# Performance work log

Measured on AMD Instinct MI355X. Metric: run time of the kernel, lower is better.

The kernel has to match this reference:

```python
import jax, jax.numpy as jnp
import numpy as np

H, N, L, BATCH = 128, 64, 4096, 8


def _make_dplr_hippo(n):
    # HiPPO-LegS -> NPLR -> DPLR diagonalization (float64 numpy, as in torch source)
    ar = np.arange(n, dtype=np.float64)
    p0 = np.sqrt(1.0 + 2.0 * ar)
    A = p0[:, None] * p0[None, :]
    A = np.tril(A) - np.diag(ar)
    nhippo = -A
    Pv = np.sqrt(ar + 0.5)
    Bv = np.sqrt(2.0 * ar + 1.0)
    S = nhippo + Pv[:, None] * Pv[None, :]
    Lambda_real = np.mean(np.diag(S)) * np.ones(n)
    Lambda_imag, V = np.linalg.eigh(S * -1j)
    V = V.astype(np.complex64)
    P = (V.conj().T @ Pv.astype(np.complex64))
    B = (V.conj().T @ Bv.astype(np.complex64))
    Lam = (Lambda_real + 1j * Lambda_imag).astype(np.complex64)
    return Lam, P, B


def _ri(x):  # complex -> [..., 2] real view (like torch.view_as_real)
    return np.stack([x.real, x.imag], axis=-1).astype(np.float32)


def setup_inputs() -> dict:
    key = jax.random.key(0)
    k_u, k_c, k_d = jax.random.split(key, 3)
    Lam, P, B = _make_dplr_hippo(N)
    Lambda_ri = np.tile(_ri(Lam)[None], (H, 1, 1))          # [H, N, 2]
    P_ri = np.tile(_ri(P)[None], (H, 1, 1))                 # [H, N, 2]
    B_ri = np.tile(_ri(B)[None], (H, 1, 1))                 # [H, N, 2]
    C_ri = jax.random.normal(k_c, (H, N, 2), dtype=jnp.float32)
    D = jax.random.normal(k_d, (H, 1), dtype=jnp.float32)
    u = jax.random.normal(k_u, (BATCH, L, H), dtype=jnp.float32)
    step = jnp.array([1.0 / L], dtype=jnp.float32)
    return {
        "u": u,
        "B_ri": jnp.asarray(B_ri),
        "C_ri": jnp.asarray(C_ri),
        "D": D,
        "Lambda_ri": jnp.asarray(Lambda_ri),
        "P_ri": jnp.asarray(P_ri),
        "step": step,
    }


def _as_c(x_ri):
    return jax.lax.complex(x_ri[..., 0], x_ri[..., 1])


def reference(u, B_ri, C_ri, D, Lambda_ri, P_ri, step):
    Bc = _as_c(B_ri)        # [H, N] complex64
    Cc = _as_c(C_ri)        # [H, N]
    Lam = _as_c(Lambda_ri)  # [H, N]
    Pc = _as_c(P_ri)        # [H, N]
    batch, seq_len, h = u.shape

    # roots of unity and bilinear-transform terms
    z = jnp.exp(-2j * jnp.pi * jnp.arange(seq_len) / seq_len)   # [L] complex64
    g = (2.0 / step).astype(jnp.complex64) * ((1.0 - z) / (1.0 + z))  # [L]
    c = 2.0 / (1.0 + z)                                          # [L]

    # Cauchy resolvent, shared by the four cauchy_dot reductions: [H, L, N]
    r = 1.0 / (g[None, :, None] - Lam[:, None, :])

    def cauchy(v):  # v: [H, N] -> [H, L]
        return jnp.einsum("hn,hln->hl", v, r)

    k00 = cauchy(jnp.conj(Cc) * Bc)
    k01 = cauchy(jnp.conj(Cc) * Pc)
    k10 = cauchy(jnp.conj(Pc) * Bc)
    k11 = cauchy(jnp.conj(Pc) * Pc)
    at_roots = c[None, :] * (k00 - k01 * (1.0 / (1.0 + k11)) * k10)  # [H, L]

    kernel = jnp.fft.ifft(at_roots, n=seq_len, axis=-1).real  # [H, L] float32

    # linear (full) FFT convolution, length 2L-1, keep first L samples
    nfft = 2 * seq_len - 1
    u_f = jnp.fft.rfft(u, n=nfft, axis=1)                 # [B, F, H]
    k_f = jnp.fft.rfft(kernel, n=nfft, axis=-1)           # [H, F]
    y = jnp.fft.irfft(u_f * k_f.T[None], n=nfft, axis=1)[:, :seq_len, :]  # [B, L, H]

    return y + u @ D  # D: [H,1] -> broadcast add of skip term
```

## Files before the change

kernel.cpp:

```cpp
#include <hip/hip_runtime.h>
#include <hip/hip_bf16.h>
#include <math.h>

#define HH 128
#define NN 64
#define LL 4096
#define BB 8
#define NFFT 8192
#define KSTR 4160

#define CAU_BLOCKS 1024
#define TRU_BLOCKS 4096
#define SKP_BLOCKS 8192

__device__ __forceinline__ float2 cmul(float2 a, float2 b) {
    return make_float2(a.x * b.x - a.y * b.y, a.x * b.y + a.y * b.x);
}
__device__ __forceinline__ float2 cadd(float2 a, float2 b) {
    return make_float2(a.x + b.x, a.y + b.y);
}
__device__ __forceinline__ float2 csub(float2 a, float2 b) {
    return make_float2(a.x - b.x, a.y - b.y);
}
__device__ __forceinline__ int brev13(int x) { return (int)(__brev((unsigned)x) >> 19); }
__device__ __forceinline__ int kkmap(int t) {
    return (t < 4096) ? (((t & 63) << 6) | (t >> 6)) : 4096;
}
__device__ __forceinline__ int swz(int v) { return v ^ ((v >> 4) & 15); }

__device__ __forceinline__ float2 twid(float rev, float sg) {
    return make_float2(__builtin_amdgcn_cosf(rev), sg * __builtin_amdgcn_sinf(rev));
}


template <int M>
__device__ __forceinline__ void dif_f8(float2* d, int N, int tid, int nt, float sg) {
    const float inv2m = 1.0f / (2.0f * (float)M);
    const float inv4m = 1.0f / (4.0f * (float)M);
    const float inv8m = 1.0f / (8.0f * (float)M);
    const float s2 = 0.70710678118654752f;
    for (int q = tid; q < (N >> 3); q += nt) {
        int j = q & (M - 1);
        int i0 = ((q & ~(M - 1)) << 3) + j;
        float2 x0 = d[swz(i0)],         x1 = d[swz(i0 + M)],
               x2 = d[swz(i0 + 2 * M)], x3 = d[swz(i0 + 3 * M)],
               x4 = d[swz(i0 + 4 * M)], x5 = d[swz(i0 + 5 * M)],
               x6 = d[swz(i0 + 6 * M)], x7 = d[swz(i0 + 7 * M)];
        float jf = (float)j;
        float2 w8 = twid(jf * inv8m, sg);
        float2 w4 = twid(jf * inv4m, sg);
        float2 w2 = twid(jf * inv2m, sg);
        float2 e1 = make_float2(s2, sg * s2);
        float2 e3 = make_float2(-s2, sg * s2);
        float2 y0 = cadd(x0, x4), y1 = cadd(x1, x5), y2 = cadd(x2, x6), y3 = cadd(x3, x7);
        float2 t0 = csub(x0, x4), t1 = csub(x1, x5), t2 = csub(x2, x6), t3 = csub(x3, x7);
        float2 w8i = make_float2(-sg * w8.y, sg * w8.x);
        float2 z0 = cmul(w8, t0);
        float2 z1 = cmul(cmul(w8, e1), t1);
        float2 z2 = cmul(w8i, t2);
        float2 z3 = cmul(cmul(w8, e3), t3);
        {
            float2 a0 = cadd(y0, y2);
            float2 a2 = cmul(w4, csub(y0, y2));
            float2 a1 = cadd(y1, y3);
            float2 t = cmul(w4, csub(y1, y3));
            float2 a3 = make_float2(-sg * t.y, sg * t.x);
            d[swz(i0)]         = cadd(a0, a1);
            d[swz(i0 + M)]     = cmul(w2, csub(a0, a1));
            d[swz(i0 + 2 * M)] = cadd(a2, a3);
            d[swz(i0 + 3 * M)] = cmul(w2, csub(a2, a3));
        }
        {
            float2 a0 = cadd(z0, z2);
            float2 a2 = cmul(w4, csub(z0, z2));
            float2 a1 = cadd(z1, z3);
            float2 t = cmul(w4, csub(z1, z3));
            float2 a3 = make_float2(-sg * t.y, sg * t.x);
            d[swz(i0 + 4 * M)] = cadd(a0, a1);
            d[swz(i0 + 5 * M)] = cmul(w2, csub(a0, a1));
            d[swz(i0 + 6 * M)] = cadd(a2, a3);
            d[swz(i0 + 7 * M)] = cmul(w2, csub(a2, a3));
        }
    }
    __syncthreads();
}

template <int M>
__device__ __forceinline__ void dit_f8(float2* d, int N, int tid, int nt, float sg) {
    const float inv2m = 1.0f / (2.0f * (float)M);
    const float inv4m = 1.0f / (4.0f * (float)M);
    const float inv8m = 1.0f / (8.0f * (float)M);
    const float s2 = 0.70710678118654752f;
    for (int q = tid; q < (N >> 3); q += nt) {
        int j = q & (M - 1);
        int i0 = ((q & ~(M - 1)) << 3) + j;
        float2 x0 = d[swz(i0)],         x1 = d[swz(i0 + M)],
               x2 = d[swz(i0 + 2 * M)], x3 = d[swz(i0 + 3 * M)],
               x4 = d[swz(i0 + 4 * M)], x5 = d[swz(i0 + 5 * M)],
               x6 = d[swz(i0 + 6 * M)], x7 = d[swz(i0 + 7 * M)];
        float jf = (float)j;
        float2 wA = twid(jf * inv2m, sg);
        float2 wB = twid(jf * inv4m, sg);
        float2 wC = twid(jf * inv8m, sg);
        float2 t;
        t = cmul(wA, x1); float2 b0 = cadd(x0, t), b1 = csub(x0, t);
        t = cmul(wA, x3); float2 b2 = cadd(x2, t), b3 = csub(x2, t);
        t = cmul(wA, x5); float2 b4 = cadd(x4, t), b5 = csub(x4, t);
        t = cmul(wA, x7); float2 b6 = cadd(x6, t), b7 = csub(x6, t);
        float2 wBi = make_float2(-sg * wB.y, sg * wB.x);
        t = cmul(wB, b2);  float2 c0 = cadd(b0, t), c2 = csub(b0, t);
        t = cmul(wBi, b3); float2 c1 = cadd(b1, t), c3 = csub(b1, t);
        t = cmul(wB, b6);  float2 c4 = cadd(b4, t), c6 = csub(b4, t);
        t = cmul(wBi, b7); float2 c5 = cadd(b5, t), c7 = csub(b5, t);
        float2 e1 = make_float2(s2, sg * s2);
        float2 e3 = make_float2(-s2, sg * s2);
        float2 w1 = cmul(wC, e1);
        float2 w2_ = make_float2(-sg * wC.y, sg * wC.x);
        float2 w3 = cmul(wC, e3);
        t = cmul(wC, c4);  d[swz(i0)]         = cadd(c0, t); d[swz(i0 + 4 * M)] = csub(c0, t);
        t = cmul(w1, c5);  d[swz(i0 + M)]     = cadd(c1, t); d[swz(i0 + 5 * M)] = csub(c1, t);
        t = cmul(w2_, c6); d[swz(i0 + 2 * M)] = cadd(c2, t); d[swz(i0 + 6 * M)] = csub(c2, t);
        t = cmul(w3, c7);  d[swz(i0 + 3 * M)] = cadd(c3, t); d[swz(i0 + 7 * M)] = csub(c3, t);
    }
    __syncthreads();
}

__global__ __launch_bounds__(256, 8) void stage1_kernel(
    const float* __restrict__ u,
    const float* __restrict__ B_ri, const float* __restrict__ C_ri,
    const float* __restrict__ D,
    const float* __restrict__ Lambda_ri, const float* __restrict__ P_ri,
    const float* __restrict__ step,
    float2* __restrict__ at_g, float* __restrict__ ut, float* __restrict__ skip) {
    __shared__ float4 smem4[264];
    const int bid = blockIdx.x;
    const int tid = threadIdx.x;

    if (bid < CAU_BLOCKS) {
        const int h = bid >> 3;
        if (tid < NN) {
            int n = tid;
            float2 C = ((const float2*)C_ri)[h * NN + n];
            float2 Bv = ((const float2*)B_ri)[h * NN + n];
            float2 P = ((const float2*)P_ri)[h * NN + n];
            float2 lam = ((const float2*)Lambda_ri)[h * NN + n];
            float2 Cc = make_float2(C.x, -C.y);
            float2 Pc = make_float2(P.x, -P.y);
            float2 v00 = cmul(Cc, Bv);
            float2 v01 = cmul(Cc, P);
            float2 v10 = cmul(Pc, Bv);
            float2 v11 = cmul(Pc, P);
            smem4[n * 3 + 0] = make_float4(lam.x, lam.y, v00.x, v00.y);
            smem4[n * 3 + 1] = make_float4(v01.x, v01.y, v10.x, v10.y);
            smem4[n * 3 + 2] = make_float4(v11.x, v11.y, 0.f, 0.f);
        }
        __syncthreads();

        const int lbase = ((bid & 7) << 8) | tid;
        const float two_over_step = 2.0f / step[0];
        float gr[2], gi[2], ccx[2], ccy[2];
#pragma unroll
        for (int p = 0; p < 2; ++p) {
            int l = lbase + p * 2048;
            double th = -6.283185307179586476925286766559 * (double)l / (double)LL;
            float sn, cs;
            sincosf((float)th, &sn, &cs);
            float dr = 1.0f + cs, di = sn;
            float inv = __builtin_amdgcn_rcpf(dr * dr + di * di);
            float nr = 1.0f - cs, ni = -sn;
            gr[p] = two_over_step * (nr * dr + ni * di) * inv;
            gi[p] = two_over_step * (ni * dr - nr * di) * inv;
            ccx[p] = 2.0f * dr * inv;
            ccy[p] = -2.0f * di * inv;
        }

        float2 k00[2], k01[2], k10[2], k11[2];
#pragma unroll
        for (int p = 0; p < 2; ++p) {
            k00[p] = make_float2(0.f, 0.f);
            k01[p] = make_float2(0.f, 0.f);
            k10[p] = make_float2(0.f, 0.f);
            k11[p] = make_float2(0.f, 0.f);
        }
#pragma unroll 4
        for (int n = 0; n < NN; ++n) {
            float4 tA = smem4[n * 3 + 0];
            float4 tB = smem4[n * 3 + 1];
            float4 tC = smem4[n * 3 + 2];
#pragma unroll
            for (int p = 0; p < 2; ++p) {
                float ar = gr[p] - tA.x, ai = gi[p] - tA.y;
                float id = __builtin_amdgcn_rcpf(ar * ar + ai * ai);
                float2 r = make_float2(ar * id, -ai * id);
                k00[p] = cadd(k00[p], cmul(make_float2(tA.z, tA.w), r));
                k01[p] = cadd(k01[p], cmul(make_float2(tB.x, tB.y), r));
                k10[p] = cadd(k10[p], cmul(make_float2(tB.z, tB.w), r));
                k11[p] = cadd(k11[p], cmul(make_float2(tC.x, tC.y), r));
            }
        }
#pragma unroll
        for (int p = 0; p < 2; ++p) {
            float wr = 1.0f + k11[p].x, wi = k11[p].y;
            float iw = __builtin_amdgcn_rcpf(wr * wr + wi * wi);
            float2 winv = make_float2(wr * iw, -wi * iw);
            float2 t = cmul(cmul(k01[p], winv), k10[p]);
            float2 at = cmul(make_float2(ccx[p], ccy[p]),
                             make_float2(k00[p].x - t.x, k00[p].y - t.y));
            at_g[(size_t)h * LL + lbase + p * 2048] = at;
        }
    } else if (bid < CAU_BLOCKS + TRU_BLOCKS) {
        float* tile = (float*)smem4;
        int tb = bid - CAU_BLOCKS;
        int b = tb >> 9;
        int h0 = ((tb >> 7) & 3) * 32;
        int l0 = (tb & 127) * 32;
        int tx = tid & 31, ty = tid >> 5;
        const float* up = u + (size_t)b * LL * HH;
        float* utp = ut + (size_t)b * HH * LL;
        for (int i = ty; i < 32; i += 8)
            tile[i * 33 + tx] = up[(size_t)(l0 + i) * HH + h0 + tx];
        __syncthreads();
        for (int i = ty; i < 32; i += 8)
            utp[(size_t)(h0 + i) * LL + l0 + tx] = tile[tx * 33 + i];
    } else {
        int sb = bid - (CAU_BLOCKS + TRU_BLOCKS);
        int wid = tid >> 6, lane = tid & 63;
        int row = sb * 4 + wid;
        const float* ur = u + (size_t)row * HH;
        float v = ur[lane] * D[lane] + ur[lane + 64] * D[lane + 64];
        for (int off = 32; off > 0; off >>= 1) v += __shfl_down(v, off, 64);
        if (lane == 0) skip[row] = v;
    }
}

__global__ __launch_bounds__(1024) void kfreq_kernel(const float2* __restrict__ at_g,
                                                     float2* __restrict__ KfP) {
    __shared__ float2 sm[NFFT];
    const int h = blockIdx.x;
    const int tid = threadIdx.x;
    const float2* ap = at_g + (size_t)h * LL;
#pragma unroll
    for (int it = 0; it < 4; ++it) {
        int t = tid + it * 1024;
        int l = ((t & 63) << 6) | (t >> 6);
        sm[swz((int)(__brev((unsigned)l) >> 20))] = ap[l];
    }
    __syncthreads();

    dit_f8<1>(sm, 4096, tid, 1024, +1.f);
    dit_f8<8>(sm, 4096, tid, 1024, +1.f);
    dit_f8<64>(sm, 4096, tid, 1024, +1.f);
    dit_f8<512>(sm, 4096, tid, 1024, +1.f);

    const float inv8192 = 1.0f / 8192.0f;
    for (int t = tid; t < 4096; t += 1024) {
        float kv = sm[swz(t)].x * (1.0f / 4096.0f);
        float2 w = twid((float)t * inv8192, -1.f);
        sm[swz(t)] = make_float2(kv, 0.f);
        sm[swz(t + 4096)] = make_float2(kv * w.x, kv * w.y);
    }
    __syncthreads();

    dif_f8<512>(sm, 8192, tid, 1024, -1.f);
    dif_f8<64>(sm, 8192, tid, 1024, -1.f);
    dif_f8<8>(sm, 8192, tid, 1024, -1.f);
    dif_f8<1>(sm, 8192, tid, 1024, -1.f);

    float2* kfp = KfP + (size_t)h * KSTR;
    for (int t = tid; t <= 4096; t += 1024) kfp[t] = sm[swz(brev13(kkmap(t)))];
}

__global__ __launch_bounds__(1024) void conv_fft_kernel(const float* __restrict__ ut,
                                                        const float2* __restrict__ KfP,
                                                        float* __restrict__ yt) {
    __shared__ float2 sm[NFFT];
    const int b = blockIdx.x >> 6;
    const int c = blockIdx.x & 63;
    const int h0 = 2 * c, h1 = 2 * c + 1;
    const int tid = threadIdx.x;
    const float* up0 = ut + ((size_t)b * HH + h0) * LL;
    const float* up1 = ut + ((size_t)b * HH + h1) * LL;
    const float inv8192 = 1.0f / 8192.0f;

    for (int i = tid; i < 4096; i += 1024) {
        float2 a = make_float2(up0[i], up1[i]);
        float2 w = twid((float)i * inv8192, -1.f);
        sm[swz(i)] = a;
        sm[swz(i + 4096)] = cmul(w, a);
    }
    __syncthreads();

    dif_f8<512>(sm, 8192, tid, 1024, -1.f);
    dif_f8<64>(sm, 8192, tid, 1024, -1.f);
    dif_f8<8>(sm, 8192, tid, 1024, -1.f);
    dif_f8<1>(sm, 8192, tid, 1024, -1.f);

    const float2* kf0 = KfP + (size_t)h0 * KSTR;
    const float2* kf1 = KfP + (size_t)h1 * KSTR;
    for (int t = tid; t <= 4096; t += 1024) {
        int kk = kkmap(t);
        bool self = (kk == 0) || (kk == 4096);
        int p = swz(brev13(kk));
        int q = self ? p : swz(brev13(NFFT - kk));
        float2 K0 = kf0[t];
        float2 K1 = kf1[t];
        float2 Zp = sm[p];
        float2 Zq = sm[q];
        float2 U0 = make_float2(0.5f * (Zp.x + Zq.x), 0.5f * (Zp.y - Zq.y));
        float2 U1 = make_float2(0.5f * (Zp.y + Zq.y), 0.5f * (Zq.x - Zp.x));
        float2 A = cmul(U0, K0);
        float2 C = cmul(U1, K1);
        sm[p] = make_float2(A.x - C.y, A.y + C.x);
        if (!self) sm[q] = make_float2(A.x + C.y, C.x - A.y);
    }
    __syncthreads();

    dit_f8<1>(sm, 8192, tid, 1024, +1.f);
    dit_f8<8>(sm, 8192, tid, 1024, +1.f);
    dit_f8<64>(sm, 8192, tid, 1024, +1.f);
    dit_f8<512>(sm, 8192, tid, 1024, +1.f);

    float* yp0 = yt + ((size_t)b * HH + h0) * LL;
    float* yp1 = yt + ((size_t)b * HH + h1) * LL;
    const float invN = 1.0f / (float)NFFT;
    for (int x = tid; x < 4096; x += 1024) {
        float2 w = twid((float)x * inv8192, +1.f);
        float2 a = sm[swz(x)];
        float2 bb = cmul(w, sm[swz(x + 4096)]);
        yp0[x] = (a.x + bb.x) * invN;
        yp1[x] = (a.y + bb.y) * invN;
    }
}

__global__ __launch_bounds__(256) void transpose_y_kernel(const float* __restrict__ yt,
                                                          const float* __restrict__ skip,
                                                          float* __restrict__ y) {
    __shared__ float tile[32][33];
    int b = blockIdx.z;
    int h0 = blockIdx.x * 32, l0 = blockIdx.y * 32;
    const float* ytp = yt + (size_t)b * HH * LL;
    const float* skp = skip + (size_t)b * LL;
    float* yp = y + (size_t)b * LL * HH;
    for (int i = threadIdx.y; i < 32; i += 8)
        tile[i][threadIdx.x] = ytp[(size_t)(h0 + i) * LL + l0 + threadIdx.x];
    __syncthreads();
    for (int i = threadIdx.y; i < 32; i += 8) {
        size_t idx = (size_t)(l0 + i) * HH + h0 + threadIdx.x;
        yp[idx] = tile[threadIdx.x][i] + skp[l0 + i];
    }
}

extern "C" void kernel_launch(void* const* d_in, const int* in_sizes, int n_in,
                              void* d_out, int out_size, void* d_ws, size_t ws_size,
                              hipStream_t stream) {
    const float* u = (const float*)d_in[0];
    const float* B_ri = (const float*)d_in[1];
    const float* C_ri = (const float*)d_in[2];
    const float* D = (const float*)d_in[3];
    const float* Lambda_ri = (const float*)d_in[4];
    const float* P_ri = (const float*)d_in[5];
    const float* step = (const float*)d_in[6];
    float* out = (float*)d_out;

    char* ws = (char*)d_ws;
    float2* KfP = (float2*)ws;
    float* skip = (float*)(ws + (size_t)6 * 1024 * 1024);
    float* ut = (float*)(ws + (size_t)8 * 1024 * 1024);
    float* yt = (float*)(ws + (size_t)24 * 1024 * 1024);
    float2* at_g = (float2*)yt;

    stage1_kernel<<<dim3(CAU_BLOCKS + TRU_BLOCKS + SKP_BLOCKS), dim3(256), 0, stream>>>(
        u, B_ri, C_ri, D, Lambda_ri, P_ri, step, at_g, ut, skip);
    kfreq_kernel<<<dim3(HH), dim3(1024), 0, stream>>>(at_g, KfP);
    conv_fft_kernel<<<dim3(BB * HH / 2), dim3(1024), 0, stream>>>(ut, KfP, yt);
    transpose_y_kernel<<<dim3(HH / 32, LL / 32, BB), dim3(32, 8), 0, stream>>>(yt, skip, out);
}
```

Before: 83.43 us.

## Fuse skip into transpose blocks, interleave u channel pairs, store conv output in fp16

The skip dot product (u @ D) is now computed inside the transpose blocks as four partial sums per row, which removes the separate skip blocks and their second read of u. The transposed input is written as interleaved float2 channel pairs, so the conv kernel loads with a single vector read. The conv output is stored as half2 instead of float32, halving the intermediate traffic to the final transpose, which sums the skip partials there. The fp16 intermediate reduces the precision of y and could exceed the error tolerance.

```diff
diff --git a/kernel.cpp b/kernel.cpp
--- a/kernel.cpp
+++ b/kernel.cpp
@@ -1,5 +1,6 @@
 #include <hip/hip_runtime.h>
 #include <hip/hip_bf16.h>
+#include <hip/hip_fp16.h>
 #include <math.h>
 
 #define HH 128
@@ -11,7 +12,6 @@
 
 #define CAU_BLOCKS 1024
 #define TRU_BLOCKS 4096
-#define SKP_BLOCKS 8192
 
 __device__ __forceinline__ float2 cmul(float2 a, float2 b) {
     return make_float2(a.x * b.x - a.y * b.y, a.x * b.y + a.y * b.x);
@@ -131,7 +131,7 @@
     const float* __restrict__ D,
     const float* __restrict__ Lambda_ri, const float* __restrict__ P_ri,
     const float* __restrict__ step,
-    float2* __restrict__ at_g, float* __restrict__ ut, float* __restrict__ skip) {
+    float2* __restrict__ at_g, float2* __restrict__ ut2, float* __restrict__ skipP) {
     __shared__ float4 smem4[264];
     const int bid = blockIdx.x;
     const int tid = threadIdx.x;
@@ -208,28 +208,34 @@
                              make_float2(k00[p].x - t.x, k00[p].y - t.y));
             at_g[(size_t)h * LL + lbase + p * 2048] = at;
         }
-    } else if (bid < CAU_BLOCKS + TRU_BLOCKS) {
+    } else {
         float* tile = (float*)smem4;
         int tb = bid - CAU_BLOCKS;
         int b = tb >> 9;
-        int h0 = ((tb >> 7) & 3) * 32;
+        int hq = (tb >> 7) & 3;
+        int h0 = hq * 32;
         int l0 = (tb & 127) * 32;
         int tx = tid & 31, ty = tid >> 5;
         const float* up = u + (size_t)b * LL * HH;
-        float* utp = ut + (size_t)b * HH * LL;
         for (int i = ty; i < 32; i += 8)
             tile[i * 33 + tx] = up[(size_t)(l0 + i) * HH + h0 + tx];
         __syncthreads();
-        for (int i = ty; i < 32; i += 8)
-            utp[(size_t)(h0 + i) * LL + l0 + tx] = tile[tx * 33 + i];
-    } else {
-        int sb = bid - (CAU_BLOCKS + TRU_BLOCKS);
-        int wid = tid >> 6, lane = tid & 63;
-        int row = sb * 4 + wid;
-        const float* ur = u + (size_t)row * HH;
-        float v = ur[lane] * D[lane] + ur[lane + 64] * D[lane + 64];
-        for (int off = 32; off > 0; off >>= 1) v += __shfl_down(v, off, 64);
-        if (lane == 0) skip[row] = v;
+        float2* utp = ut2 + (size_t)b * 64 * LL;
+#pragma unroll
+        for (int i = ty; i < 16; i += 8) {
+            int c = (h0 >> 1) + i;
+            float2 v = make_float2(tile[tx * 33 + 2 * i], tile[tx * 33 + 2 * i + 1]);
+            utp[(size_t)c * LL + l0 + tx] = v;
+        }
+        int llocal = tid >> 3, g = tid & 7;
+        float s = 0.f;
+#pragma unroll
+        for (int k = 0; k < 4; ++k)
+            s += tile[llocal * 33 + g * 4 + k] * D[h0 + g * 4 + k];
+        s += __shfl_down(s, 4, 8);
+        s += __shfl_down(s, 2, 8);
+        s += __shfl_down(s, 1, 8);
+        if (g == 0) skipP[((size_t)b * 4 + hq) * LL + l0 + llocal] = s;
     }
 }
 
@@ -270,20 +276,19 @@
     for (int t = tid; t <= 4096; t += 1024) kfp[t] = sm[swz(brev13(kkmap(t)))];
 }
 
-__global__ __launch_bounds__(1024) void conv_fft_kernel(const float* __restrict__ ut,
+__global__ __launch_bounds__(1024) void conv_fft_kernel(const float2* __restrict__ ut2,
                                                         const float2* __restrict__ KfP,
-                                                        float* __restrict__ yt) {
+                                                        __half2* __restrict__ yt2) {
     __shared__ float2 sm[NFFT];
     const int b = blockIdx.x >> 6;
     const int c = blockIdx.x & 63;
     const int h0 = 2 * c, h1 = 2 * c + 1;
     const int tid = threadIdx.x;
-    const float* up0 = ut + ((size_t)b * HH + h0) * LL;
-    const float* up1 = ut + ((size_t)b * HH + h1) * LL;
+    const float2* up2 = ut2 + ((size_t)b * 64 + c) * LL;
     const float inv8192 = 1.0f / 8192.0f;
 
     for (int i = tid; i < 4096; i += 1024) {
-        float2 a = make_float2(up0[i], up1[i]);
+        float2 a = up2[i];
         float2 w = twid((float)i * inv8192, -1.f);
         sm[swz(i)] = a;
         sm[swz(i + 4096)] = cmul(w, a);
@@ -320,33 +325,37 @@
     dit_f8<64>(sm, 8192, tid, 1024, +1.f);
     dit_f8<512>(sm, 8192, tid, 1024, +1.f);
 
-    float* yp0 = yt + ((size_t)b * HH + h0) * LL;
-    float* yp1 = yt + ((size_t)b * HH + h1) * LL;
+    __half2* yp = yt2 + ((size_t)b * 64 + c) * LL;
     const float invN = 1.0f / (float)NFFT;
     for (int x = tid; x < 4096; x += 1024) {
         float2 w = twid((float)x * inv8192, +1.f);
         float2 a = sm[swz(x)];
         float2 bb = cmul(w, sm[swz(x + 4096)]);
-        yp0[x] = (a.x + bb.x) * invN;
-        yp1[x] = (a.y + bb.y) * invN;
-    }
-}
-
-__global__ __launch_bounds__(256) void transpose_y_kernel(const float* __restrict__ yt,
-                                                          const float* __restrict__ skip,
+        yp[x] = __floats2half2_rn((a.x + bb.x) * invN, (a.y + bb.y) * invN);
+    }
+}
+
+__global__ __launch_bounds__(256) void transpose_y_kernel(const __half2* __restrict__ yt2,
+                                                          const float* __restrict__ skipP,
                                                           float* __restrict__ y) {
-    __shared__ float tile[32][33];
+    __shared__ __half2 tile[32 * 17];
     int b = blockIdx.z;
-    int h0 = blockIdx.x * 32, l0 = blockIdx.y * 32;
-    const float* ytp = yt + (size_t)b * HH * LL;
-    const float* skp = skip + (size_t)b * LL;
+    int c0 = blockIdx.x * 16;
+    int l0 = blockIdx.y * 32;
+    int tx = threadIdx.x, ty = threadIdx.y;
+    const __half2* ytp = yt2 + (size_t)b * 64 * LL;
+    const float* skp = skipP + (size_t)b * 4 * LL;
     float* yp = y + (size_t)b * LL * HH;
-    for (int i = threadIdx.y; i < 32; i += 8)
-        tile[i][threadIdx.x] = ytp[(size_t)(h0 + i) * LL + l0 + threadIdx.x];
-    __syncthreads();
-    for (int i = threadIdx.y; i < 32; i += 8) {
-        size_t idx = (size_t)(l0 + i) * HH + h0 + threadIdx.x;
-        yp[idx] = tile[threadIdx.x][i] + skp[l0 + i];
+    for (int i = ty; i < 16; i += 8)
+        tile[tx * 17 + i] = ytp[(size_t)(c0 + i) * LL + l0 + tx];
+    __syncthreads();
+    int h0 = c0 * 2;
+    for (int i = ty; i < 32; i += 8) {
+        int l = l0 + i;
+        float sk = skp[l] + skp[LL + l] + skp[2 * LL + l] + skp[3 * LL + l];
+        float2 f = __half22float2(tile[i * 17 + (tx >> 1)]);
+        float v = (tx & 1) ? f.y : f.x;
+        yp[(size_t)l * HH + h0 + tx] = v + sk;
     }
 }
 
@@ -364,14 +373,15 @@
 
     char* ws = (char*)d_ws;
     float2* KfP = (float2*)ws;
-    float* skip = (float*)(ws + (size_t)6 * 1024 * 1024);
-    float* ut = (float*)(ws + (size_t)8 * 1024 * 1024);
-    float* yt = (float*)(ws + (size_t)24 * 1024 * 1024);
-    float2* at_g = (float2*)yt;
-
-    stage1_kernel<<<dim3(CAU_BLOCKS + TRU_BLOCKS + SKP_BLOCKS), dim3(256), 0, stream>>>(
-        u, B_ri, C_ri, D, Lambda_ri, P_ri, step, at_g, ut, skip);
+    float* skipP = (float*)(ws + (size_t)6 * 1024 * 1024);
+    float2* ut2 = (float2*)(ws + (size_t)8 * 1024 * 1024);
+    char* hi = ws + (size_t)24 * 1024 * 1024;
+    float2* at_g = (float2*)hi;
+    __half2* yt2 = (__half2*)hi;
+
+    stage1_kernel<<<dim3(CAU_BLOCKS + TRU_BLOCKS), dim3(256), 0, stream>>>(
+        u, B_ri, C_ri, D, Lambda_ri, P_ri, step, at_g, ut2, skipP);
     kfreq_kernel<<<dim3(HH), dim3(1024), 0, stream>>>(at_g, KfP);
-    conv_fft_kernel<<<dim3(BB * HH / 2), dim3(1024), 0, stream>>>(ut, KfP, yt);
-    transpose_y_kernel<<<dim3(HH / 32, LL / 32, BB), dim3(32, 8), 0, stream>>>(yt, skip, out);
-}
+    conv_fft_kernel<<<dim3(BB * HH / 2), dim3(1024), 0, stream>>>(ut2, KfP, yt2);
+    transpose_y_kernel<<<dim3(HH / 32, LL / 32, BB), dim3(32, 8), 0, stream>>>(yt2, skipP, out);
+}
```

New measurement: 82.58 us. No clear change (-1.0%).
